# Kernel optimization log

Measured on AMD Instinct MI355X. Metric: run time of the kernel, lower is better.

## Reference

```python
import jax, jax.numpy as jnp
import numpy as np

B, S, D, H, DFF, L, VOCAB = 4, 2048, 512, 8, 2048, 6, 32000
DK = D // H


def positional_encoding(n_step, d):
    pos = jnp.arange(n_step, dtype=jnp.float32)[:, None]            # (S,1)
    i = jnp.arange(d, dtype=jnp.float32)                            # (D,)
    ang = pos * (1.0 / jnp.power(10000.0, 2.0 * jnp.floor(i / 2.0) / d))
    odd = (jnp.arange(d) % 2).astype(bool)
    return jnp.where(odd, jnp.cos(ang), jnp.sin(ang))               # (S,D)


def layer_norm(x, g, b, eps=1e-6):
    m = x.mean(-1, keepdims=True)
    v = ((x - m) ** 2).mean(-1, keepdims=True)
    return g * (x - m) * jax.lax.rsqrt(v + eps) + b


def mha(Q, K, V, Wq, bq, Wo, bo, mask):
    # Faithful to source: Wq is (buggily) used for Q, K and V projections.
    def split(t):
        return t.reshape(t.shape[0], -1, H, DK).transpose(0, 2, 1, 3)  # (B,H,S,dk)
    q = split(Q @ Wq + bq)
    k = split(K @ Wq + bq)
    v = split(V @ Wq + bq)
    scores = jnp.einsum('bhqd,bhkd->bhqk', q, k) / jnp.sqrt(jnp.float32(DK))
    if mask is not None:
        scores = scores + mask * (-1e9)
    attn = jax.nn.softmax(scores, axis=-1)
    out = jnp.einsum('bhqk,bhkd->bhqd', attn, v)
    out = out.transpose(0, 2, 1, 3).reshape(Q.shape[0], -1, D)
    return out @ Wo + bo


def setup_inputs() -> dict:
    key = jax.random.key(0)
    ks = jax.random.split(key, 16)
    inputs = jax.random.randint(ks[0], (B, S), 0, VOCAB)
    enc_inputs = jax.random.normal(ks[1], (B, S, D), dtype=jnp.float32)
    # causal mask (1 = masked) broadcast over heads, per source mask*-1e9 convention
    comb = 1.0 - jnp.tril(jnp.ones((S, S), dtype=jnp.float32))
    comb_mask = jnp.broadcast_to(comb, (B, 1, S, S))
    padding_mask = jnp.zeros((B, 1, 1, S), dtype=jnp.float32)
    s = 0.02
    emb = jax.random.normal(ks[2], (VOCAB, D), dtype=jnp.float32) * s
    Wq1 = jax.random.normal(ks[3], (L, D, D), dtype=jnp.float32) * s
    bq1 = jnp.zeros((L, D), dtype=jnp.float32)
    Wo1 = jax.random.normal(ks[4], (L, D, D), dtype=jnp.float32) * s
    bo1 = jnp.zeros((L, D), dtype=jnp.float32)
    Wq2 = jax.random.normal(ks[5], (L, D, D), dtype=jnp.float32) * s
    bq2 = jnp.zeros((L, D), dtype=jnp.float32)
    Wo2 = jax.random.normal(ks[6], (L, D, D), dtype=jnp.float32) * s
    bo2 = jnp.zeros((L, D), dtype=jnp.float32)
    W1 = jax.random.normal(ks[7], (L, D, DFF), dtype=jnp.float32) * s
    b1 = jnp.zeros((L, DFF), dtype=jnp.float32)
    W2 = jax.random.normal(ks[8], (L, DFF, D), dtype=jnp.float32) * s
    b2 = jnp.zeros((L, D), dtype=jnp.float32)
    ln_g = jnp.ones((L, 3, D), dtype=jnp.float32)
    ln_b = jnp.zeros((L, 3, D), dtype=jnp.float32)
    return dict(inputs=inputs, enc_inputs=enc_inputs, comb_mask=comb_mask,
                padding_mask=padding_mask, emb=emb, Wq1=Wq1, bq1=bq1, Wo1=Wo1,
                bo1=bo1, Wq2=Wq2, bq2=bq2, Wo2=Wo2, bo2=bo2, W1=W1, b1=b1,
                W2=W2, b2=b2, ln_g=ln_g, ln_b=ln_b)


def reference(inputs, enc_inputs, comb_mask, padding_mask, emb, Wq1, bq1, Wo1,
              bo1, Wq2, bq2, Wo2, bo2, W1, b1, W2, b2, ln_g, ln_b):
    # embedding + sinusoidal positional encoding (dropout = identity at eval)
    x = emb[inputs] * jnp.sqrt(jnp.float32(D)) + positional_encoding(S, D)
    for l in range(L):
        a1 = mha(x, x, x, Wq1[l], bq1[l], Wo1[l], bo1[l], comb_mask)
        x1 = layer_norm(a1 + x, ln_g[l, 0], ln_b[l, 0])
        a2 = mha(x1, enc_inputs, enc_inputs, Wq2[l], bq2[l], Wo2[l], bo2[l], padding_mask)
        x2 = layer_norm(a2 + x1, ln_g[l, 1], ln_b[l, 1])
        f = jax.nn.relu(x2 @ W1[l] + b1[l]) @ W2[l] + b2[l]
        x = layer_norm(x2 + f, ln_g[l, 2], ln_b[l, 2])
    return x
```

## Files before the change

### kernel.cpp

```cpp
#include <hip/hip_runtime.h>
#include <hip/hip_bf16.h>
#include <cstddef>
#include <cstdint>

#define BB   4
#define SS   2048
#define DD   512
#define HH   8
#define DFFC 2048
#define LLC  6
#define DKH  64
#define MMR  (BB * SS)

typedef short s16x8 __attribute__((ext_vector_type(8)));
typedef float f32x4 __attribute__((ext_vector_type(4)));
typedef unsigned short us4 __attribute__((ext_vector_type(4)));
typedef unsigned int u32;

__device__ __forceinline__ unsigned short f2bf(float f) {
  union { float f; unsigned int u; } v; v.f = f;
  const unsigned int u = v.u;
  return (unsigned short)((u + 0x7FFFu + ((u >> 16) & 1u)) >> 16);
}
__device__ __forceinline__ float bflo(u32 u) { return __uint_as_float(u << 16); }
__device__ __forceinline__ float bfhi(u32 u) { return __uint_as_float(u & 0xffff0000u); }

__device__ __forceinline__ s16x8 ld8(const unsigned short* p) {
  return *(const s16x8*)p;
}

__device__ __forceinline__ void gload16(const unsigned short* g, unsigned short* l) {
  __builtin_amdgcn_global_load_lds(
      (const __attribute__((address_space(1))) void*)g,
      (__attribute__((address_space(3))) void*)l, 16, 0, 0);
}

__global__ __launch_bounds__(256) void k_embed_pe(const int* __restrict__ toks,
                                                  const float* __restrict__ emb,
                                                  unsigned short* __restrict__ xb) {
  const int t = blockIdx.x;
  const int s = t & (SS - 1);
  const int tok = toks[t];
  const float ln10k = 9.210340371976184f;
  for (int d = threadIdx.x; d < DD; d += 256) {
    const int e = d >> 1;
    const float ex = 2.0f * (float)e * (1.0f / (float)DD);
    const float freq = expf(-ex * ln10k);
    const float ang = (float)s * freq;
    const float pe = (d & 1) ? cosf(ang) : sinf(ang);
    const float v = emb[(size_t)tok * DD + d] * 22.62741699796952f + pe;
    xb[(size_t)t * DD + d] = f2bf(v);
  }
}

__global__ __launch_bounds__(256) void k_f32_to_bf16(const float* __restrict__ src,
                                                     unsigned short* __restrict__ dst) {
  const int i = (blockIdx.x * 256 + threadIdx.x) * 4;
  const float4 v = *(const float4*)(src + i);
  us4 w;
  w.x = f2bf(v.x); w.y = f2bf(v.y); w.z = f2bf(v.z); w.w = f2bf(v.w);
  *(us4*)(dst + i) = w;
}

__global__ __launch_bounds__(256) void k_wt(const float* s0, const float* s1,
                                            const float* s2, const float* s3,
                                            const float* s4, const float* s5,
                                            unsigned short* d0, unsigned short* d1,
                                            unsigned short* d2, unsigned short* d3,
                                            unsigned short* d4, unsigned short* d5) {
  const int t = blockIdx.x;
  const int tid = threadIdx.x;
  const float* src; unsigned short* dst; int K, N, tile, lntn;
  if (t < 256) {
    const int m = t >> 6; tile = t & 63; K = 512; N = 512; lntn = 3;
    src = (m == 0) ? s0 : (m == 1) ? s1 : (m == 2) ? s2 : s3;
    dst = (m == 0) ? d0 : (m == 1) ? d1 : (m == 2) ? d2 : d3;
  } else if (t < 512) {
    src = s4; dst = d4; K = 512; N = 2048; tile = t - 256; lntn = 5;
  } else {
    src = s5; dst = d5; K = 2048; N = 512; tile = t - 512; lntn = 3;
  }
  const int tn = tile & ((1 << lntn) - 1);
  const int tk = tile >> lntn;
  const int k0 = tk * 64, n0 = tn * 64;

  __shared__ unsigned short T[64][68];
#pragma unroll
  for (int i = 0; i < 4; ++i) {
    const int f = i * 256 + tid;
    const int r = f >> 4, c4 = (f & 15) << 2;
    const float4 v = *(const float4*)(src + (size_t)(k0 + r) * N + n0 + c4);
    us4 w;
    w.x = f2bf(v.x); w.y = f2bf(v.y); w.z = f2bf(v.z); w.w = f2bf(v.w);
    *(us4*)&T[r][c4] = w;
  }
  __syncthreads();
#pragma unroll
  for (int i = 0; i < 4; ++i) {
    const int f = i * 256 + tid;
    const int n = f >> 4, k4 = (f & 15) << 2;
    us4 w;
    w.x = T[k4 + 0][n]; w.y = T[k4 + 1][n];
    w.z = T[k4 + 2][n]; w.w = T[k4 + 3][n];
    *(us4*)&dst[(size_t)(n0 + n) * K + k0 + k4] = w;
  }
}

template<int BN, bool RELU, bool VT>
__global__ __launch_bounds__(256) void k_gemm_mfma(const unsigned short* __restrict__ A,
                                                   const unsigned short* __restrict__ Bt,
                                                   const float* __restrict__ bias,
                                                   unsigned short* __restrict__ Cb,
                                                   unsigned short* __restrict__ Vt,
                                                   int voff, int M, int N, int K) {
  constexpr int NT = BN / 32;
  __shared__ unsigned short As[128 * 64];
  __shared__ unsigned short Bs[BN * 64];

  const int tid = threadIdx.x;
  const int wave = tid >> 6, lane = tid & 63;
  const int quad = lane >> 4, l16 = lane & 15;
  const int wm = wave & 1, wn = wave >> 1;
  const int mbase = blockIdx.x * 128, nbase = blockIdx.y * BN;

  f32x4 acc[4][NT];
#pragma unroll
  for (int mt = 0; mt < 4; ++mt)
#pragma unroll
    for (int nt = 0; nt < NT; ++nt) acc[mt][nt] = (f32x4){0.f, 0.f, 0.f, 0.f};

  for (int kb = 0; kb < K; kb += 64) {
    __syncthreads();
#pragma unroll
    for (int i = 0; i < 4; ++i) {
      const int c = i * 256 + wave * 64 + lane;
      const int m = c >> 3;
      const int k8 = (c & 7) ^ (m & 7);
      gload16(A + (size_t)(mbase + m) * K + kb + k8 * 8,
              As + (size_t)(i * 256 + wave * 64) * 8);
    }
#pragma unroll
    for (int i = 0; i < BN / 32; ++i) {
      const int c = i * 256 + wave * 64 + lane;
      const int n = c >> 3;
      const int k8 = (c & 7) ^ (n & 7);
      gload16(Bt + (size_t)(nbase + n) * K + kb + k8 * 8,
              Bs + (size_t)(i * 256 + wave * 64) * 8);
    }
    __syncthreads();
#pragma unroll
    for (int kh = 0; kh < 2; ++kh) {
      s16x8 af[4];
#pragma unroll
      for (int mt = 0; mt < 4; ++mt) {
        const int m = wm * 64 + mt * 16 + l16;
        const int cc = m * 8 + ((kh * 4 + quad) ^ (m & 7));
        af[mt] = ld8(As + cc * 8);
      }
#pragma unroll
      for (int nt = 0; nt < NT; ++nt) {
        const int n = wn * (BN / 2) + nt * 16 + l16;
        const int cc = n * 8 + ((kh * 4 + quad) ^ (n & 7));
        const s16x8 bf = ld8(Bs + cc * 8);
#pragma unroll
        for (int mt = 0; mt < 4; ++mt)
          acc[mt][nt] = __builtin_amdgcn_mfma_f32_16x16x32_bf16(af[mt], bf, acc[mt][nt], 0, 0, 0);
      }
    }
  }

#pragma unroll
  for (int nt = 0; nt < NT; ++nt) {
    const int col = nbase + wn * (BN / 2) + nt * 16 + l16;
    const float bv = bias[col];
#pragma unroll
    for (int mt = 0; mt < 4; ++mt) {
      const int row0 = mbase + wm * 64 + mt * 16 + quad * 4;
      float vv[4];
#pragma unroll
      for (int r = 0; r < 4; ++r) {
        float v = acc[mt][nt][r] + bv;
        if (RELU) v = fmaxf(v, 0.0f);
        vv[r] = v;
        Cb[(size_t)(row0 + r) * N + col] = f2bf(v);
      }
      if (VT) {
        if (row0 >= voff) {
          const int vrow = row0 - voff;
          const int bb = vrow >> 11, s0 = vrow & 2047;
          us4 o;
          o.x = f2bf(vv[0]); o.y = f2bf(vv[1]); o.z = f2bf(vv[2]); o.w = f2bf(vv[3]);
          *(us4*)(Vt + ((size_t)((bb * 8 + (col >> 6)) * 64 + (col & 63))) * SS + s0) = o;
        }
      }
    }
  }
}

__global__ __launch_bounds__(512, 4) void k_attn_mfma(const unsigned short* __restrict__ Qp,
                                                      const unsigned short* __restrict__ Kp,
                                                      const unsigned short* __restrict__ Vtp,
                                                      unsigned short* __restrict__ Out,
                                                      int causal) {
  __shared__ __align__(16) unsigned char smem[53248];
  unsigned short* KsB = (unsigned short*)smem;
  unsigned short* VsB = (unsigned short*)(smem + 16384);
  unsigned short* PsB = (unsigned short*)(smem + 32768);

  const int hb = blockIdx.x;
  const int h = hb & 7, b = hb >> 3;
  const int by = blockIdx.y;
  const int qt = causal ? ((by < 8) ? (15 - by) : (by - 8)) : by;
  const int tid = threadIdx.x;
  const int w = tid >> 6, lane = tid & 63;
  const int quad = lane >> 4, l16 = lane & 15;
  const int qg = w & 3, ks = w >> 2;

  s16x8 aq[2][2];
#pragma unroll
  for (int mt = 0; mt < 2; ++mt) {
    const int qrow = b * SS + qt * 128 + qg * 32 + mt * 16 + l16;
#pragma unroll
    for (int kh = 0; kh < 2; ++kh) {
      s16x8 v = *(const s16x8*)(Qp + (size_t)qrow * DD + h * DKH + kh * 32 + quad * 8);
#pragma unroll
      for (int j = 0; j < 8; ++j) {
        const unsigned int u = ((unsigned int)(unsigned short)v[j]) << 16;
        const float f = __uint_as_float(u) * 0.125f;
        v[j] = (short)(unsigned short)(__float_as_uint(f) >> 16);
      }
      aq[mt][kh] = v;
    }
  }

  f32x4 O[2][4];
  float l_r[2][4];
#pragma unroll
  for (int mt = 0; mt < 2; ++mt)
#pragma unroll
    for (int i = 0; i < 4; ++i) { O[mt][i] = (f32x4){0.f, 0.f, 0.f, 0.f}; l_r[mt][i] = 0.f; }

  const unsigned short* Kb = Kp + (size_t)(b * SS) * DD + h * DKH;
  const unsigned short* Vb = Vtp + (size_t)hb * DKH * SS;

  const int nkt = causal ? (2 * qt + 2) : (SS / 64);

  auto stage = [&](int kt2, int buf) {
    const int r = tid >> 3, c8 = tid & 7;
    gload16(Kb + (size_t)(kt2 * 64 + r) * DD + ((c8 ^ (r & 7)) << 3),
            KsB + buf * 4096 + w * 512);
    gload16(Vb + (size_t)r * SS + kt2 * 64 + ((c8 ^ (r & 7)) << 3),
            VsB + buf * 4096 + w * 512);
  };

  unsigned short* Psw = PsB + w * 32 * 40;

  stage(0, 0);
  for (int kt = 0; kt < nkt; ++kt) {
    __syncthreads();
    if (kt + 1 < nkt) stage(kt + 1, (kt + 1) & 1);
    const unsigned short* ksp = KsB + (kt & 1) * 4096;
    const unsigned short* vsp = VsB + (kt & 1) * 4096;

    f32x4 S[2][2];
#pragma unroll
    for (int nt = 0; nt < 2; ++nt) {
      const int key = ks * 32 + nt * 16 + l16;
      const s16x8 b0 = ld8(ksp + (key * 8 + (quad ^ (key & 7))) * 8);
      const s16x8 b1 = ld8(ksp + (key * 8 + ((4 + quad) ^ (key & 7))) * 8);
#pragma unroll
      for (int mt = 0; mt < 2; ++mt) {
        f32x4 s = (f32x4){0.f, 0.f, 0.f, 0.f};
        s = __builtin_amdgcn_mfma_f32_16x16x32_bf16(aq[mt][0], b0, s, 0, 0, 0);
        s = __builtin_amdgcn_mfma_f32_16x16x32_bf16(aq[mt][1], b1, s, 0, 0, 0);
        S[mt][nt] = s;
      }
    }

    s16x8 vb[4];
#pragma unroll
    for (int nt = 0; nt < 4; ++nt) {
      const int d = nt * 16 + l16;
      vb[nt] = ld8(vsp + (d * 8 + ((ks * 4 + quad) ^ (d & 7))) * 8);
    }

#pragma unroll
    for (int mt = 0; mt < 2; ++mt) {
      const int qb = qt * 128 + qg * 32 + mt * 16;
      const bool needmask = causal && (kt * 64 + 63 > qb);
#pragma unroll
      for (int nt = 0; nt < 2; ++nt) {
#pragma unroll
        for (int r = 0; r < 4; ++r) {
          float p = __expf(S[mt][nt][r]);
          if (needmask) {
            const int key = kt * 64 + ks * 32 + nt * 16 + l16;
            if (key > qb + quad * 4 + r) p = 0.0f;
          }
          const unsigned int pu = __float_as_uint(p) & 0xffff0000u;
          l_r[mt][r] += __uint_as_float(pu);
          Psw[(mt * 16 + quad * 4 + r) * 40 + nt * 16 + l16] = (unsigned short)(pu >> 16);
        }
      }
    }
    asm volatile("s_waitcnt lgkmcnt(0)" ::: "memory");

    s16x8 ap[2];
    ap[0] = ld8(Psw + (l16) * 40 + quad * 8);
    ap[1] = ld8(Psw + (16 + l16) * 40 + quad * 8);
#pragma unroll
    for (int nt = 0; nt < 4; ++nt)
#pragma unroll
      for (int mt = 0; mt < 2; ++mt)
        O[mt][nt] = __builtin_amdgcn_mfma_f32_16x16x32_bf16(ap[mt], vb[nt], O[mt][nt], 0, 0, 0);
  }

  float lr[2][4];
#pragma unroll
  for (int mt = 0; mt < 2; ++mt)
#pragma unroll
    for (int r = 0; r < 4; ++r) {
      float l = l_r[mt][r];
      l += __shfl_xor(l, 1);
      l += __shfl_xor(l, 2);
      l += __shfl_xor(l, 4);
      l += __shfl_xor(l, 8);
      lr[mt][r] = l;
    }

  __syncthreads();
  float* Obuf = (float*)smem;
  float* Lbuf = (float*)(smem + 33792);
  if (ks == 1) {
#pragma unroll
    for (int mt = 0; mt < 2; ++mt)
#pragma unroll
      for (int r = 0; r < 4; ++r) {
        const int row = qg * 32 + mt * 16 + quad * 4 + r;
        if (l16 == 0) Lbuf[row] = lr[mt][r];
#pragma unroll
        for (int nt = 0; nt < 4; ++nt)
          Obuf[(size_t)row * 66 + nt * 16 + l16] = O[mt][nt][r];
      }
  }
  __syncthreads();
  if (ks == 0) {
#pragma unroll
    for (int mt = 0; mt < 2; ++mt)
#pragma unroll
      for (int r = 0; r < 4; ++r) {
        const int row = qg * 32 + mt * 16 + quad * 4 + r;
        const float linv = 1.0f / (lr[mt][r] + Lbuf[row]);
        unsigned short* orow = Out + (size_t)(b * SS + qt * 128 + row) * DD + h * DKH;
#pragma unroll
        for (int nt = 0; nt < 4; ++nt)
          orow[nt * 16 + l16] = f2bf((O[mt][nt][r] + Obuf[(size_t)row * 66 + nt * 16 + l16]) * linv);
      }
  }
}

__device__ __forceinline__ float block_reduce_sum(float v) {
  __shared__ float red[4];
#pragma unroll
  for (int off = 32; off > 0; off >>= 1) v += __shfl_down(v, off);
  const int lane = threadIdx.x & 63;
  const int w = threadIdx.x >> 6;
  __syncthreads();
  if (lane == 0) red[w] = v;
  __syncthreads();
  return red[0] + red[1] + red[2] + red[3];
}

template<bool F32OUT>
__global__ __launch_bounds__(256) void k_add_ln(const unsigned short* __restrict__ a,
                                                const unsigned short* __restrict__ r,
                                                const float* __restrict__ g,
                                                const float* __restrict__ be,
                                                unsigned short* __restrict__ ob,
                                                float* __restrict__ of) {
  const int row = blockIdx.x;
  const int t = threadIdx.x;
  const size_t base = (size_t)row * DD + t * 2;
  const u32 av = *(const u32*)(a + base);
  const u32 rv = *(const u32*)(r + base);
  const float v0 = bflo(av) + bflo(rv);
  const float v1 = bfhi(av) + bfhi(rv);
  const float s = block_reduce_sum(v0 + v1);
  const float mean = s * (1.0f / (float)DD);
  const float d0 = v0 - mean;
  const float d1 = v1 - mean;
  const float var = block_reduce_sum(d0 * d0 + d1 * d1) * (1.0f / (float)DD);
  const float inv = rsqrtf(var + 1e-6f);
  const float o0 = g[t * 2] * d0 * inv + be[t * 2];
  const float o1 = g[t * 2 + 1] * d1 * inv + be[t * 2 + 1];
  const u32 o = (u32)f2bf(o0) | ((u32)f2bf(o1) << 16);
  *(u32*)(ob + base) = o;
  if (F32OUT) {
    of[base]     = o0;
    of[base + 1] = o1;
  }
}

extern "C" void kernel_launch(void* const* d_in, const int* in_sizes, int n_in,
                              void* d_out, int out_size, void* d_ws, size_t ws_size,
                              hipStream_t stream) {
  const int*   toks = (const int*)d_in[0];
  const float* enc  = (const float*)d_in[1];
  const float* emb  = (const float*)d_in[4];
  const float* Wq1  = (const float*)d_in[5];
  const float* bq1  = (const float*)d_in[6];
  const float* Wo1  = (const float*)d_in[7];
  const float* bo1  = (const float*)d_in[8];
  const float* Wq2  = (const float*)d_in[9];
  const float* bq2  = (const float*)d_in[10];
  const float* Wo2  = (const float*)d_in[11];
  const float* bo2  = (const float*)d_in[12];
  const float* W1   = (const float*)d_in[13];
  const float* b1   = (const float*)d_in[14];
  const float* W2   = (const float*)d_in[15];
  const float* b2   = (const float*)d_in[16];
  const float* lng  = (const float*)d_in[17];
  const float* lnb  = (const float*)d_in[18];
  float* out = (float*)d_out;

  char* p = (char*)d_ws;
  unsigned short* Wq1t = (unsigned short*)p; p += (size_t)512 * 512 * 2;
  unsigned short* Wo1t = (unsigned short*)p; p += (size_t)512 * 512 * 2;
  unsigned short* Wq2t = (unsigned short*)p; p += (size_t)512 * 512 * 2;
  unsigned short* Wo2t = (unsigned short*)p; p += (size_t)512 * 512 * 2;
  unsigned short* W1t  = (unsigned short*)p; p += (size_t)2048 * 512 * 2;
  unsigned short* W2t  = (unsigned short*)p; p += (size_t)512 * 2048 * 2;
  unsigned short* Xcur = (unsigned short*)p; p += (size_t)MMR * DD * 2;
  unsigned short* Cat  = (unsigned short*)p; p += (size_t)2 * MMR * DD * 2;
  unsigned short* Pm   = (unsigned short*)p; p += (size_t)2 * MMR * DD * 2;
  unsigned short* Ab   = (unsigned short*)p; p += (size_t)MMR * DD * 2;
  unsigned short* Gb   = (unsigned short*)p; p += (size_t)MMR * DD * 2;
  unsigned short* X2b  = (unsigned short*)p; p += (size_t)MMR * DD * 2;
  unsigned short* Vt   = (unsigned short*)p; p += (size_t)MMR * DD * 2;
  unsigned short* Hb   = (unsigned short*)p; p += (size_t)MMR * DFFC * 2;
  unsigned short* encb = Cat + (size_t)MMR * DD;

  const dim3 blk(256);
  const dim3 blkA(512);
  const dim3 gP(MMR / 128, DD / 64);
  const dim3 gM(2 * MMR / 128, DD / 64);
  const dim3 gF1(MMR / 128, DFFC / 128);
  const dim3 gAttn(HH * BB, SS / 128);

  k_embed_pe<<<MMR, blk, 0, stream>>>(toks, emb, Xcur);
  k_f32_to_bf16<<<(MMR * DD) / 1024, blk, 0, stream>>>(enc, encb);

  for (int l = 0; l < LLC; ++l) {
    const float* wq1 = Wq1 + (size_t)l * DD * DD;
    const float* wo1 = Wo1 + (size_t)l * DD * DD;
    const float* wq2 = Wq2 + (size_t)l * DD * DD;
    const float* wo2 = Wo2 + (size_t)l * DD * DD;
    const float* w1  = W1  + (size_t)l * DD * DFFC;
    const float* w2  = W2  + (size_t)l * DFFC * DD;
    const float* bq1l = bq1 + (size_t)l * DD;
    const float* bo1l = bo1 + (size_t)l * DD;
    const float* bq2l = bq2 + (size_t)l * DD;
    const float* bo2l = bo2 + (size_t)l * DD;
    const float* b1l  = b1  + (size_t)l * DFFC;
    const float* b2l  = b2  + (size_t)l * DD;
    const float* g0 = lng + ((size_t)l * 3 + 0) * DD;
    const float* e0 = lnb + ((size_t)l * 3 + 0) * DD;
    const float* g1 = lng + ((size_t)l * 3 + 1) * DD;
    const float* e1 = lnb + ((size_t)l * 3 + 1) * DD;
    const float* g2 = lng + ((size_t)l * 3 + 2) * DD;
    const float* e2 = lnb + ((size_t)l * 3 + 2) * DD;

    k_wt<<<768, blk, 0, stream>>>(wq1, wo1, wq2, wo2, w1, w2,
                                  Wq1t, Wo1t, Wq2t, Wo2t, W1t, W2t);

    k_gemm_mfma<64, false, true><<<gP, blk, 0, stream>>>(Xcur, Wq1t, bq1l, Pm, Vt, 0, MMR, DD, DD);
    k_attn_mfma<<<gAttn, blkA, 0, stream>>>(Pm, Pm, Vt, Ab, 1);
    k_gemm_mfma<64, false, false><<<gP, blk, 0, stream>>>(Ab, Wo1t, bo1l, Gb, nullptr, 0, MMR, DD, DD);
    k_add_ln<false><<<MMR, blk, 0, stream>>>(Gb, Xcur, g0, e0, Cat, nullptr);

    k_gemm_mfma<64, false, true><<<gM, blk, 0, stream>>>(Cat, Wq2t, bq2l, Pm, Vt, MMR, 2 * MMR, DD, DD);
    k_attn_mfma<<<gAttn, blkA, 0, stream>>>(Pm, Pm + (size_t)MMR * DD, Vt, Ab, 0);
    k_gemm_mfma<64, false, false><<<gP, blk, 0, stream>>>(Ab, Wo2t, bo2l, Gb, nullptr, 0, MMR, DD, DD);
    k_add_ln<false><<<MMR, blk, 0, stream>>>(Gb, Cat, g1, e1, X2b, nullptr);

    k_gemm_mfma<128, true, false><<<gF1, blk, 0, stream>>>(X2b, W1t, b1l, Hb, nullptr, 0, MMR, DFFC, DD);
    k_gemm_mfma<64, false, false><<<gP, blk, 0, stream>>>(Hb, W2t, b2l, Gb, nullptr, 0, MMR, DD, DFFC);
    if (l == LLC - 1)
      k_add_ln<true><<<MMR, blk, 0, stream>>>(Gb, X2b, g2, e2, Xcur, out);
    else
      k_add_ln<false><<<MMR, blk, 0, stream>>>(Gb, X2b, g2, e2, Xcur, nullptr);
  }
}
```

Before: 1.633 ms.

## Keep attention probabilities in registers via transposed QK^T MFMA, drop LDS P staging

Computes S transposed (K fragments as the A operand, Q as B), so each lane's softmax outputs already sit in the A-operand layout needed by the PV MFMA. The probabilities are packed to bf16 with v_cvt_pk_bf16_f32 directly into registers, which removes the per-warp LDS round trip for P and its waitcnt. V fragments are gathered as two 4-element halves to match the new key ordering. The row-sum reduction changes to cross-quad shuffles. Shared memory shrinks, the occupancy hint goes to 8 blocks, and MFMA sections get s_setprio. Rounding of P changes from truncation to round-to-nearest, and the raised occupancy target may cause register spilling.

```diff
diff --git a/kernel.cpp b/kernel.cpp
--- a/kernel.cpp
+++ b/kernel.cpp
@@ -13,9 +13,11 @@
 #define MMR  (BB * SS)
 
 typedef short s16x8 __attribute__((ext_vector_type(8)));
+typedef short s16x4 __attribute__((ext_vector_type(4)));
 typedef float f32x4 __attribute__((ext_vector_type(4)));
 typedef unsigned short us4 __attribute__((ext_vector_type(4)));
 typedef unsigned int u32;
+typedef unsigned int u32x4 __attribute__((ext_vector_type(4)));
 
 __device__ __forceinline__ unsigned short f2bf(float f) {
   union { float f; unsigned int u; } v; v.f = f;
@@ -27,6 +29,12 @@
 
 __device__ __forceinline__ s16x8 ld8(const unsigned short* p) {
   return *(const s16x8*)p;
+}
+
+__device__ __forceinline__ u32 cvtpk(float a, float b) {
+  u32 r;
+  asm("v_cvt_pk_bf16_f32 %0, %1, %2" : "=v"(r) : "v"(a), "v"(b));
+  return r;
 }
 
 __device__ __forceinline__ void gload16(const unsigned short* g, unsigned short* l) {
@@ -197,15 +205,14 @@
   }
 }
 
-__global__ __launch_bounds__(512, 4) void k_attn_mfma(const unsigned short* __restrict__ Qp,
+__global__ __launch_bounds__(512, 8) void k_attn_mfma(const unsigned short* __restrict__ Qp,
                                                       const unsigned short* __restrict__ Kp,
                                                       const unsigned short* __restrict__ Vtp,
                                                       unsigned short* __restrict__ Out,
                                                       int causal) {
-  __shared__ __align__(16) unsigned char smem[53248];
+  __shared__ __align__(16) unsigned char smem[34816];
   unsigned short* KsB = (unsigned short*)smem;
   unsigned short* VsB = (unsigned short*)(smem + 16384);
-  unsigned short* PsB = (unsigned short*)(smem + 32768);
 
   const int hb = blockIdx.x;
   const int h = hb & 7, b = hb >> 3;
@@ -234,11 +241,13 @@
   }
 
   f32x4 O[2][4];
-  float l_r[2][4];
-#pragma unroll
-  for (int mt = 0; mt < 2; ++mt)
-#pragma unroll
-    for (int i = 0; i < 4; ++i) { O[mt][i] = (f32x4){0.f, 0.f, 0.f, 0.f}; l_r[mt][i] = 0.f; }
+  float l_r[2];
+#pragma unroll
+  for (int mt = 0; mt < 2; ++mt) {
+    l_r[mt] = 0.f;
+#pragma unroll
+    for (int i = 0; i < 4; ++i) O[mt][i] = (f32x4){0.f, 0.f, 0.f, 0.f};
+  }
 
   const unsigned short* Kb = Kp + (size_t)(b * SS) * DD + h * DKH;
   const unsigned short* Vb = Vtp + (size_t)hb * DKH * SS;
@@ -253,8 +262,6 @@
             VsB + buf * 4096 + w * 512);
   };
 
-  unsigned short* Psw = PsB + w * 32 * 40;
-
   stage(0, 0);
   for (int kt = 0; kt < nkt; ++kt) {
     __syncthreads();
@@ -262,71 +269,87 @@
     const unsigned short* ksp = KsB + (kt & 1) * 4096;
     const unsigned short* vsp = VsB + (kt & 1) * 4096;
 
+    s16x8 kf[2][2];
+#pragma unroll
+    for (int kg = 0; kg < 2; ++kg) {
+      const int row = ks * 32 + kg * 16 + l16;
+#pragma unroll
+      for (int kh = 0; kh < 2; ++kh)
+        kf[kg][kh] = ld8(ksp + (row * 8 + ((kh * 4 + quad) ^ (row & 7))) * 8);
+    }
+
     f32x4 S[2][2];
-#pragma unroll
-    for (int nt = 0; nt < 2; ++nt) {
-      const int key = ks * 32 + nt * 16 + l16;
-      const s16x8 b0 = ld8(ksp + (key * 8 + (quad ^ (key & 7))) * 8);
-      const s16x8 b1 = ld8(ksp + (key * 8 + ((4 + quad) ^ (key & 7))) * 8);
-#pragma unroll
-      for (int mt = 0; mt < 2; ++mt) {
+    __builtin_amdgcn_s_setprio(1);
+#pragma unroll
+    for (int mt = 0; mt < 2; ++mt)
+#pragma unroll
+      for (int kg = 0; kg < 2; ++kg) {
         f32x4 s = (f32x4){0.f, 0.f, 0.f, 0.f};
-        s = __builtin_amdgcn_mfma_f32_16x16x32_bf16(aq[mt][0], b0, s, 0, 0, 0);
-        s = __builtin_amdgcn_mfma_f32_16x16x32_bf16(aq[mt][1], b1, s, 0, 0, 0);
-        S[mt][nt] = s;
-      }
-    }
-
-    s16x8 vb[4];
+        s = __builtin_amdgcn_mfma_f32_16x16x32_bf16(kf[kg][0], aq[mt][0], s, 0, 0, 0);
+        s = __builtin_amdgcn_mfma_f32_16x16x32_bf16(kf[kg][1], aq[mt][1], s, 0, 0, 0);
+        S[mt][kg] = s;
+      }
+    __builtin_amdgcn_s_setprio(0);
+
+    s16x8 vbf[4];
 #pragma unroll
     for (int nt = 0; nt < 4; ++nt) {
       const int d = nt * 16 + l16;
-      vb[nt] = ld8(vsp + (d * 8 + ((ks * 4 + quad) ^ (d & 7))) * 8);
-    }
-
+      const int ch = ks * 4 + (quad >> 1);
+      const int hof = (quad & 1) * 4;
+      const s16x4 g1 = *(const s16x4*)(vsp + d * 64 + ((ch ^ (d & 7)) * 8) + hof);
+      const s16x4 g2 = *(const s16x4*)(vsp + d * 64 + (((ch + 2) ^ (d & 7)) * 8) + hof);
+      vbf[nt] = __builtin_shufflevector(g1, g2, 0, 1, 2, 3, 4, 5, 6, 7);
+    }
+
+    s16x8 pa[2];
 #pragma unroll
     for (int mt = 0; mt < 2; ++mt) {
       const int qb = qt * 128 + qg * 32 + mt * 16;
       const bool needmask = causal && (kt * 64 + 63 > qb);
-#pragma unroll
-      for (int nt = 0; nt < 2; ++nt) {
+      const int q = qb + l16;
+      float pv[2][4];
+#pragma unroll
+      for (int kg = 0; kg < 2; ++kg) {
 #pragma unroll
         for (int r = 0; r < 4; ++r) {
-          float p = __expf(S[mt][nt][r]);
+          float p = __expf(S[mt][kg][r]);
           if (needmask) {
-            const int key = kt * 64 + ks * 32 + nt * 16 + l16;
-            if (key > qb + quad * 4 + r) p = 0.0f;
+            const int key = kt * 64 + ks * 32 + kg * 16 + quad * 4 + r;
+            if (key > q) p = 0.0f;
           }
-          const unsigned int pu = __float_as_uint(p) & 0xffff0000u;
-          l_r[mt][r] += __uint_as_float(pu);
-          Psw[(mt * 16 + quad * 4 + r) * 40 + nt * 16 + l16] = (unsigned short)(pu >> 16);
+          pv[kg][r] = p;
         }
       }
-    }
-    asm volatile("s_waitcnt lgkmcnt(0)" ::: "memory");
-
-    s16x8 ap[2];
-    ap[0] = ld8(Psw + (l16) * 40 + quad * 8);
-    ap[1] = ld8(Psw + (16 + l16) * 40 + quad * 8);
+      l_r[mt] += ((pv[0][0] + pv[0][1]) + (pv[0][2] + pv[0][3]))
+               + ((pv[1][0] + pv[1][1]) + (pv[1][2] + pv[1][3]));
+      u32x4 pk;
+      pk.x = cvtpk(pv[0][0], pv[0][1]);
+      pk.y = cvtpk(pv[0][2], pv[0][3]);
+      pk.z = cvtpk(pv[1][0], pv[1][1]);
+      pk.w = cvtpk(pv[1][2], pv[1][3]);
+      pa[mt] = __builtin_bit_cast(s16x8, pk);
+    }
+
+    __builtin_amdgcn_s_setprio(1);
 #pragma unroll
     for (int nt = 0; nt < 4; ++nt)
 #pragma unroll
       for (int mt = 0; mt < 2; ++mt)
-        O[mt][nt] = __builtin_amdgcn_mfma_f32_16x16x32_bf16(ap[mt], vb[nt], O[mt][nt], 0, 0, 0);
-  }
-
-  float lr[2][4];
-#pragma unroll
-  for (int mt = 0; mt < 2; ++mt)
-#pragma unroll
-    for (int r = 0; r < 4; ++r) {
-      float l = l_r[mt][r];
-      l += __shfl_xor(l, 1);
-      l += __shfl_xor(l, 2);
-      l += __shfl_xor(l, 4);
-      l += __shfl_xor(l, 8);
-      lr[mt][r] = l;
-    }
+        O[mt][nt] = __builtin_amdgcn_mfma_f32_16x16x32_bf16(pa[mt], vbf[nt], O[mt][nt], 0, 0, 0);
+    __builtin_amdgcn_s_setprio(0);
+  }
+
+  float lq[2][4];
+#pragma unroll
+  for (int mt = 0; mt < 2; ++mt) {
+    float l = l_r[mt];
+    l += __shfl_xor(l, 16);
+    l += __shfl_xor(l, 32);
+#pragma unroll
+    for (int r = 0; r < 4; ++r)
+      lq[mt][r] = __shfl(l, quad * 4 + r);
+  }
 
   __syncthreads();
   float* Obuf = (float*)smem;
@@ -337,7 +360,7 @@
 #pragma unroll
       for (int r = 0; r < 4; ++r) {
         const int row = qg * 32 + mt * 16 + quad * 4 + r;
-        if (l16 == 0) Lbuf[row] = lr[mt][r];
+        if (l16 == 0) Lbuf[row] = lq[mt][r];
 #pragma unroll
         for (int nt = 0; nt < 4; ++nt)
           Obuf[(size_t)row * 66 + nt * 16 + l16] = O[mt][nt][r];
@@ -350,7 +373,7 @@
 #pragma unroll
       for (int r = 0; r < 4; ++r) {
         const int row = qg * 32 + mt * 16 + quad * 4 + r;
-        const float linv = 1.0f / (lr[mt][r] + Lbuf[row]);
+        const float linv = 1.0f / (lq[mt][r] + Lbuf[row]);
         unsigned short* orow = Out + (size_t)(b * SS + qt * 128 + row) * DD + h * DKH;
 #pragma unroll
         for (int nt = 0; nt < 4; ++nt)
```

After: 4.223 ms. 159% more time.
